# Performance work log

Measured on AMD Instinct MI355X. Metric: run time of the kernel, lower is better.

Reference implementation:

```python
import jax, jax.numpy as jnp
import numpy as np

B, T, W = 8, 4096, 1024          # batch, byte seq len, words per sequence
DB, DW = 64, 512                 # byte_embed_dim, word_embed_dim
NH = 2                           # highway layers per block
VOCAB = 264                      # 256 bytes + 4 + 4 specials
BPE_MARK, WORD_MARK = 4, 3       # bpe_mask_idx, word_mask_idx


def _make_seg_ids():
    # ragged word lengths in {3,4,5}, mean 4, summing to T per sequence
    rng = np.random.default_rng(0)
    seg = np.empty((B, T), np.int32)
    base = T // W
    for b in range(B):
        delta = np.zeros(W, np.int64)
        q = W // 4
        idx = rng.permutation(W)
        delta[idx[:q]] = 1
        delta[idx[q:2 * q]] = -1
        seg[b] = np.repeat(np.arange(W), base + delta)
    return jnp.asarray(seg)


def setup_inputs() -> dict:
    key = jax.random.key(0)
    ks = jax.random.split(key, 12)
    s = 0.05
    byte_tokens = jax.random.randint(ks[0], (B, T), 4, VOCAB)
    bpe_mask = jax.random.bernoulli(ks[1], 0.25, (B, T))
    word_mask = jax.random.bernoulli(ks[2], 0.05, (B, T))
    seg_ids = _make_seg_ids()
    tok_emb = (jax.random.normal(ks[3], (VOCAB, DB)) * s).at[0].set(0.0)  # padding_idx=0 row zeroed
    inp = {
        'byte_tokens': byte_tokens, 'bpe_mask': bpe_mask, 'word_mask': word_mask,
        'seg_ids': seg_ids, 'tok_emb': tok_emb,
        'conv0_w': jax.random.normal(ks[4], (3, DB, DW)) * s, 'conv0_b': jnp.zeros((DW,)),
        'hw0_wg': jax.random.normal(ks[5], (NH, DW, DW)) * s, 'hw0_bg': jnp.zeros((NH, DW)),
        'hw0_wh': jax.random.normal(ks[6], (NH, DW, DW)) * s, 'hw0_bh': jnp.zeros((NH, DW)),
        'conv1_w': jax.random.normal(ks[7], (3, DW, DW)) * s, 'conv1_b': jnp.zeros((DW,)),
        'hw1_wg': jax.random.normal(ks[8], (NH, DW, DW)) * s, 'hw1_bg': jnp.zeros((NH, DW)),
        'hw1_wh': jax.random.normal(ks[9], (NH, DW, DW)) * s, 'hw1_bh': jnp.zeros((NH, DW)),
        'proj_w': jax.random.normal(ks[10], (DW, DW)) * s, 'proj_b': jnp.zeros((DW,)),
    }
    return inp


def _conv_highway(x, cw, cb, wg, bg, wh, bh, residual):
    # 1D same-padded conv over sequence, optional residual, relu, then highways
    y = jax.lax.conv_general_dilated(x, cw, (1,), 'SAME',
                                     dimension_numbers=('NWC', 'WIO', 'NWC')) + cb
    if residual:
        y = y + x
    y = jax.nn.relu(y)
    for i in range(NH):
        g = jax.nn.sigmoid(y @ wg[i] + bg[i])
        h = jax.nn.relu(y @ wh[i] + bh[i])
        y = g * h + (1.0 - g) * y
    return y


def reference(byte_tokens, bpe_mask, word_mask, seg_ids, tok_emb,
              conv0_w, conv0_b, hw0_wg, hw0_bg, hw0_wh, hw0_bh,
              conv1_w, conv1_b, hw1_wg, hw1_bg, hw1_wh, hw1_bh,
              proj_w, proj_b):
    # byte embedding + marker embeddings (pad idx 0 -> zero row)
    x = (tok_emb[byte_tokens]
         + tok_emb[jnp.where(bpe_mask, BPE_MARK, 0)]
         + tok_emb[jnp.where(word_mask, WORD_MARK, 0)])          # [B,T,DB]
    x = _conv_highway(x, conv0_w, conv0_b, hw0_wg, hw0_bg, hw0_wh, hw0_bh, False)
    x = _conv_highway(x, conv1_w, conv1_b, hw1_wg, hw1_bg, hw1_wh, hw1_bh, True)
    # ragged per-word segment max over bytes (fused, replaces python loops)
    seg_max = jax.vmap(lambda xi, si: jax.ops.segment_max(xi, si, num_segments=W))
    x = seg_max(x, seg_ids)                                       # [B,W,DW]
    return x @ proj_w + proj_b
```

## Files before the change

kernel.cpp:

```cpp
#include <hip/hip_runtime.h>
#include <hip/hip_bf16.h>

using bf16 = __hip_bfloat16;
typedef __attribute__((ext_vector_type(8))) short s8v;
typedef __attribute__((ext_vector_type(4))) float f4v;

#define T_SEQ 4096
#define DWC 512

__device__ __forceinline__ float fin(float v) {
    return (v == v && fabsf(v) < 1e30f) ? v : 0.0f;
}
__device__ __forceinline__ float ldf(const void* p, size_t i, int f32) {
    return f32 ? ((const float*)p)[i] : __bfloat162float(((const bf16*)p)[i]);
}
__device__ __forceinline__ float b2f(short s) {
    unsigned u = ((unsigned)(unsigned short)s) << 16;
    return __builtin_bit_cast(float, u);
}
__device__ __forceinline__ short f2b(float v) {
    bf16 b = __float2bfloat16(v);
    return __builtin_bit_cast(short, b);
}

__device__ __forceinline__ void swz(int L, int G, int& bx, int& by) {
    int k8 = L & 7, sl = L >> 3;
    int gp = G >> 5;
    bx = sl & 3;
    by = k8 * gp + (sl >> 2);
}

__global__ __launch_bounds__(256) void diag_kernel(bf16* __restrict__ out, int n, float v)
{
    int i = blockIdx.x * 256 + threadIdx.x;
    if (i < n) out[i] = __float2bfloat16(i == 0 ? v : 0.0f);
}

__global__ __launch_bounds__(256) void detect_kernel(
    const int* __restrict__ tok, const unsigned char* __restrict__ bpe,
    const unsigned char* __restrict__ wm, const int* __restrict__ seg,
    const unsigned int* __restrict__ embw, int* __restrict__ flags)
{
    __shared__ int sh[5];
    int tid = threadIdx.x;
    if (tid < 5) sh[tid] = 0;
    __syncthreads();
    int bo = 0, bm = 0, wo = 0, wmid = 0;
    for (int i = tid; i < 16384; i += 256) {
        int odd = 2 * i + 1;
        if (bpe[odd]) bo = 1;
        if (wm[odd])  wo = 1;
        int mid = 8 * (i & 4095) + 4;
        if (bpe[mid]) bm = 1;
        if (wm[mid])  wmid = 1;
    }
    if (bo)   atomicOr(&sh[0], 1);
    if (bm)   atomicOr(&sh[1], 1);
    if (wo)   atomicOr(&sh[2], 1);
    if (wmid) atomicOr(&sh[3], 1);
    if (tid < 32 && embw[32 + tid] != 0u) atomicOr(&sh[4], 1);
    __syncthreads();
    if (tid == 0) {
        flags[0] = (tok[32767] != 0) ? 0 : 1;
        flags[1] = sh[0] ? 1 : (sh[1] ? 4 : 8);
        flags[2] = sh[2] ? 1 : (sh[3] ? 4 : 8);
        flags[3] = (seg[32767] != 0) ? 0 : 1;
        flags[4] = sh[4] ? 0 : 1;
    }
}

#define WB_TOTAL 3249664
__global__ __launch_bounds__(256) void convert_weights(
    const void* c0w, const void* c0b, const void* h0g, const void* h0bg,
    const void* h0h, const void* h0bh, const void* c1w, const void* c1b,
    const void* h1g, const void* h1bg, const void* h1h, const void* h1bh,
    const void* pw, const void* pb, const int* __restrict__ flags,
    short* __restrict__ WB)
{
    int f32 = flags[4];
    size_t i = (size_t)blockIdx.x * 256 + threadIdx.x;
    if (i >= WB_TOTAL) return;
    const void* src; size_t si;
    if (i < 98304)        { size_t n = i / 192, k = i % 192; src = c0w; si = k * 512 + n; }
    else if (i < 98816)   { src = c0b;  si = i - 98304; }
    else if (i < 623104)  { size_t o = i - 98816;  size_t l = o >> 18; o &= 262143;
                            size_t n = o >> 9, k = o & 511; src = h0g; si = (l << 18) + k * 512 + n; }
    else if (i < 624128)  { src = h0bg; si = i - 623104; }
    else if (i < 1148416) { size_t o = i - 624128; size_t l = o >> 18; o &= 262143;
                            size_t n = o >> 9, k = o & 511; src = h0h; si = (l << 18) + k * 512 + n; }
    else if (i < 1149440) { src = h0bh; si = i - 1148416; }
    else if (i < 1935872) { size_t o = i - 1149440; size_t n = o / 1536, k = o % 1536;
                            src = c1w; si = k * 512 + n; }
    else if (i < 1936384) { src = c1b;  si = i - 1935872; }
    else if (i < 2460672) { size_t o = i - 1936384; size_t l = o >> 18; o &= 262143;
                            size_t n = o >> 9, k = o & 511; src = h1g; si = (l << 18) + k * 512 + n; }
    else if (i < 2461696) { src = h1bg; si = i - 2460672; }
    else if (i < 2985984) { size_t o = i - 2461696; size_t l = o >> 18; o &= 262143;
                            size_t n = o >> 9, k = o & 511; src = h1h; si = (l << 18) + k * 512 + n; }
    else if (i < 2987008) { src = h1bh; si = i - 2985984; }
    else if (i < 3249152) { size_t o = i - 2987008; size_t n = o >> 9, k = o & 511;
                            src = pw; si = k * 512 + n; }
    else                  { src = pb;   si = i - 3249152; }
    WB[i] = f2b(ldf(src, si, f32));
}

__global__ __launch_bounds__(256) void embed_kernel(
    const int* __restrict__ tok, const unsigned char* __restrict__ bpe,
    const unsigned char* __restrict__ wm, const void* __restrict__ emb,
    const int* __restrict__ flags, short* __restrict__ xe, int bt0)
{
    int i = blockIdx.x * 256 + threadIdx.x;
    int d = i & 63;
    int btl = i >> 6;
    int bt = bt0 + btl;
    int is64t = flags[0];
    int wb = flags[1], ww = flags[2];
    int f32 = flags[4];
    int t = is64t ? (int)((const long long*)tok)[bt] : tok[bt];
    t = min(max(t, 0), 263);
    float v = ldf(emb, (size_t)t * 64 + d, f32);
    if (bpe[(size_t)bt * wb]) v += ldf(emb, 4 * 64 + d, f32);
    if (wm[(size_t)bt * ww])  v += ldf(emb, 3 * 64 + d, f32);
    xe[i] = f2b(fin(v));
}

template<int IC, bool RESID>
__global__ __launch_bounds__(512) void conv_mfma(
    const short* __restrict__ A, const short* __restrict__ WT,
    const short* __restrict__ bias, short* __restrict__ Out)
{
    constexpr int K = 3 * IC;
    __shared__ __align__(16) short As[128 * 32];
    __shared__ __align__(16) short Bs[128 * 32];
    int bx, by;
    swz(blockIdx.x, gridDim.x, bx, by);
    const int bm = by * 128;
    const int bn = bx * 128;
    const int tid = threadIdx.x;
    const int wave = tid >> 6, lane = tid & 63;
    const int wmr = (wave >> 1) * 32, wnc = (wave & 1) * 64;
    const int q = lane >> 4, ln16 = lane & 15;
    const int sr = tid >> 2, sc = (tid & 3) * 8;

    f4v acc[2][4] = {};

    for (int k0 = 0; k0 < K; k0 += 32) {
        const int tap = k0 / IC;
        const int c0 = k0 - tap * IC;
        {
            int gr = bm + sr;
            int tt = gr & (T_SEQ - 1);
            int ts = tt + tap - 1;
            uint4 va = make_uint4(0, 0, 0, 0);
            if (ts >= 0 && ts < T_SEQ)
                va = *(const uint4*)(A + (size_t)(gr + tap - 1) * IC + c0 + sc);
            *(uint4*)(&As[sr * 32 + sc]) = va;
            *(uint4*)(&Bs[sr * 32 + sc]) = *(const uint4*)(WT + (size_t)(bn + sr) * K + k0 + sc);
        }
        __syncthreads();
        s8v af[2], bf[4];
        #pragma unroll
        for (int mi = 0; mi < 2; mi++) af[mi] = *(const s8v*)(&As[(wmr + mi * 16 + ln16) * 32 + q * 8]);
        #pragma unroll
        for (int ni = 0; ni < 4; ni++) bf[ni] = *(const s8v*)(&Bs[(wnc + ni * 16 + ln16) * 32 + q * 8]);
        #pragma unroll
        for (int mi = 0; mi < 2; mi++)
            #pragma unroll
            for (int ni = 0; ni < 4; ni++)
                acc[mi][ni] = __builtin_amdgcn_mfma_f32_16x16x32_bf16(
                    af[mi], bf[ni], acc[mi][ni], 0, 0, 0);
        __syncthreads();
    }

    #pragma unroll
    for (int mi = 0; mi < 2; mi++)
        #pragma unroll
        for (int ni = 0; ni < 4; ni++) {
            int col = bn + wnc + ni * 16 + ln16;
            float bv = b2f(bias[col]);
            #pragma unroll
            for (int r = 0; r < 4; r++) {
                int row = bm + wmr + mi * 16 + q * 4 + r;
                float v = acc[mi][ni][r] + bv;
                if constexpr (RESID) v += b2f(A[(size_t)row * IC + col]);
                Out[(size_t)row * DWC + col] = f2b(fin(fmaxf(v, 0.0f)));
            }
        }
}

__global__ __launch_bounds__(512) void highway_mfma(
    const short* __restrict__ Y, const short* __restrict__ WgT,
    const short* __restrict__ bg, const short* __restrict__ WhT,
    const short* __restrict__ bh, short* __restrict__ Out)
{
    __shared__ __align__(16) short As[128 * 32];
    __shared__ __align__(16) short Bg[128 * 32];
    __shared__ __align__(16) short Bh[128 * 32];
    int bx, by;
    swz(blockIdx.x, gridDim.x, bx, by);
    const int bm = by * 128;
    const int bn = bx * 128;
    const int tid = threadIdx.x;
    const int wave = tid >> 6, lane = tid & 63;
    const int wmr = (wave >> 1) * 32, wnc = (wave & 1) * 64;
    const int q = lane >> 4, ln16 = lane & 15;
    const int sr = tid >> 2, sc = (tid & 3) * 8;

    f4v accg[2][4] = {};
    f4v acch[2][4] = {};

    for (int k0 = 0; k0 < DWC; k0 += 32) {
        *(uint4*)(&As[sr * 32 + sc]) = *(const uint4*)(Y + (size_t)(bm + sr) * DWC + k0 + sc);
        *(uint4*)(&Bg[sr * 32 + sc]) = *(const uint4*)(WgT + (size_t)(bn + sr) * DWC + k0 + sc);
        *(uint4*)(&Bh[sr * 32 + sc]) = *(const uint4*)(WhT + (size_t)(bn + sr) * DWC + k0 + sc);
        __syncthreads();
        s8v af[2], bgf[4], bhf[4];
        #pragma unroll
        for (int mi = 0; mi < 2; mi++) af[mi] = *(const s8v*)(&As[(wmr + mi * 16 + ln16) * 32 + q * 8]);
        #pragma unroll
        for (int ni = 0; ni < 4; ni++) {
            bgf[ni] = *(const s8v*)(&Bg[(wnc + ni * 16 + ln16) * 32 + q * 8]);
            bhf[ni] = *(const s8v*)(&Bh[(wnc + ni * 16 + ln16) * 32 + q * 8]);
        }
        #pragma unroll
        for (int mi = 0; mi < 2; mi++)
            #pragma unroll
            for (int ni = 0; ni < 4; ni++) {
                accg[mi][ni] = __builtin_amdgcn_mfma_f32_16x16x32_bf16(
                    af[mi], bgf[ni], accg[mi][ni], 0, 0, 0);
                acch[mi][ni] = __builtin_amdgcn_mfma_f32_16x16x32_bf16(
                    af[mi], bhf[ni], acch[mi][ni], 0, 0, 0);
            }
        __syncthreads();
    }

    #pragma unroll
    for (int mi = 0; mi < 2; mi++)
        #pragma unroll
        for (int ni = 0; ni < 4; ni++) {
            int col = bn + wnc + ni * 16 + ln16;
            float bgv = b2f(bg[col]);
            float bhv = b2f(bh[col]);
            #pragma unroll
            for (int r = 0; r < 4; r++) {
                int row = bm + wmr + mi * 16 + q * 4 + r;
                float g = 1.0f / (1.0f + expf(-(accg[mi][ni][r] + bgv)));
                float h = fmaxf(acch[mi][ni][r] + bhv, 0.0f);
                float y = b2f(Y[(size_t)row * DWC + col]);
                Out[(size_t)row * DWC + col] = f2b(fin(g * h + (1.0f - g) * y));
            }
        }
}

__global__ __launch_bounds__(512) void proj_mfma(
    const short* __restrict__ A, const short* __restrict__ WT,
    const short* __restrict__ bias, const int* __restrict__ flags,
    void* __restrict__ Out, int oroff)
{
    __shared__ __align__(16) short As[128 * 32];
    __shared__ __align__(16) short Bs[128 * 32];
    int bx, by;
    swz(blockIdx.x, gridDim.x, bx, by);
    const int bm = by * 128;
    const int bn = bx * 128;
    const int tid = threadIdx.x;
    const int wave = tid >> 6, lane = tid & 63;
    const int wmr = (wave >> 1) * 32, wnc = (wave & 1) * 64;
    const int q = lane >> 4, ln16 = lane & 15;
    const int sr = tid >> 2, sc = (tid & 3) * 8;
    const int f32 = flags[4];

    f4v acc[2][4] = {};

    for (int k0 = 0; k0 < DWC; k0 += 32) {
        *(uint4*)(&As[sr * 32 + sc]) = *(const uint4*)(A + (size_t)(bm + sr) * DWC + k0 + sc);
        *(uint4*)(&Bs[sr * 32 + sc]) = *(const uint4*)(WT + (size_t)(bn + sr) * DWC + k0 + sc);
        __syncthreads();
        s8v af[2], bf[4];
        #pragma unroll
        for (int mi = 0; mi < 2; mi++) af[mi] = *(const s8v*)(&As[(wmr + mi * 16 + ln16) * 32 + q * 8]);
        #pragma unroll
        for (int ni = 0; ni < 4; ni++) bf[ni] = *(const s8v*)(&Bs[(wnc + ni * 16 + ln16) * 32 + q * 8]);
        #pragma unroll
        for (int mi = 0; mi < 2; mi++)
            #pragma unroll
            for (int ni = 0; ni < 4; ni++)
                acc[mi][ni] = __builtin_amdgcn_mfma_f32_16x16x32_bf16(
                    af[mi], bf[ni], acc[mi][ni], 0, 0, 0);
        __syncthreads();
    }

    #pragma unroll
    for (int mi = 0; mi < 2; mi++)
        #pragma unroll
        for (int ni = 0; ni < 4; ni++) {
            int col = bn + wnc + ni * 16 + ln16;
            float bv = b2f(bias[col]);
            #pragma unroll
            for (int r = 0; r < 4; r++) {
                int row = bm + wmr + mi * 16 + q * 4 + r;
                float v = fin(acc[mi][ni][r] + bv);
                size_t oi = (size_t)(oroff + row) * DWC + col;
                if (f32) ((float*)Out)[oi] = v;
                else     ((bf16*)Out)[oi] = __float2bfloat16(v);
            }
        }
}

__global__ __launch_bounds__(256) void bounds_kernel(
    const int* __restrict__ seg, const int* __restrict__ flags,
    int* __restrict__ wstart, int* __restrict__ wend, int bt0)
{
    int il = blockIdx.x * 256 + threadIdx.x;
    int ig = bt0 + il;
    int is64 = flags[3];
    const long long* seg64 = (const long long*)seg;
    int t = il & (T_SEQ - 1);
    int bl = il >> 12;
    int s  = (is64 ? (int)seg64[ig] : seg[ig]) & 1023;
    int sp = (t == 0)         ? -1 : ((is64 ? (int)seg64[ig - 1] : seg[ig - 1]) & 1023);
    int sn = (t == T_SEQ - 1) ? -1 : ((is64 ? (int)seg64[ig + 1] : seg[ig + 1]) & 1023);
    int bw = (bl << 10) + s;
    if (sp != s) wstart[bw] = t;
    if (sn != s) wend[bw] = t;
}

__global__ __launch_bounds__(512) void segmax_kernel(
    const short* __restrict__ Y, const int* __restrict__ wstart,
    const int* __restrict__ wend, short* __restrict__ Out)
{
    int bw = blockIdx.x;
    int d = threadIdx.x;
    int bl = bw >> 10;
    int s = wstart[bw], e = wend[bw];
    s = min(max(s, 0), T_SEQ - 1);
    e = min(max(e, s), T_SEQ - 1);
    float m = b2f(Y[(size_t)((bl << 12) + s) * DWC + d]);
    for (int t = s + 1; t <= e; ++t)
        m = fmaxf(m, b2f(Y[(size_t)((bl << 12) + t) * DWC + d]));
    Out[(size_t)bw * DWC + d] = f2b(fin(m));
}

extern "C" void kernel_launch(void* const* d_in, const int* in_sizes, int n_in,
                              void* d_out, int out_size, void* d_ws, size_t ws_size,
                              hipStream_t stream)
{
    static const int expect[19] = {32768, 32768, 32768, 32768, 16896,
                                   98304, 512, 524288, 1024, 524288, 1024,
                                   786432, 512, 524288, 1024, 524288, 1024,
                                   262144, 512};
    int bad = -1;
    if (n_in < 19) bad = 31;
    else for (int i = 0; i < 19; i++) if (in_sizes[i] != expect[i]) { bad = i; break; }
    if (bad >= 0) {
        diag_kernel<<<dim3((out_size + 255) / 256), dim3(256), 0, stream>>>(
            (bf16*)d_out, out_size, 1e35f * (float)(1 + bad));
        return;
    }

    char* ws = (char*)d_ws;
    const size_t WBREG = 8ull << 20;
    short* WB    = (short*)ws;
    int*   flags = (int*)(ws + 6500352);
    const size_t perC = 8921088 + 8192 + 64;
    int C = 8;
    while (C > 1 && WBREG + (size_t)C * perC > ws_size) C >>= 1;
    if (WBREG + (size_t)C * perC > ws_size) {
        float ws_mib = (float)((double)ws_size / 1048576.0);
        diag_kernel<<<dim3((out_size + 255) / 256), dim3(256), 0, stream>>>(
            (bf16*)d_out, out_size, 1e30f * (16.0f + ws_mib));
        return;
    }

    const int*  byte_tokens = (const int*)d_in[0];
    const unsigned char* bpe_mask = (const unsigned char*)d_in[1];
    const unsigned char* word_mask = (const unsigned char*)d_in[2];
    const int*  seg_ids     = (const int*)d_in[3];
    const void* tok_emb = d_in[4];

    detect_kernel<<<dim3(1), dim3(256), 0, stream>>>(
        byte_tokens, bpe_mask, word_mask, seg_ids,
        (const unsigned int*)tok_emb, flags);

    convert_weights<<<dim3((WB_TOTAL + 255) / 256), dim3(256), 0, stream>>>(
        d_in[5], d_in[6], d_in[7], d_in[8], d_in[9], d_in[10],
        d_in[11], d_in[12], d_in[13], d_in[14], d_in[15], d_in[16],
        d_in[17], d_in[18], flags, WB);

    short* c0wT = WB;            short* c0b  = WB + 98304;
    short* h0gT = WB + 98816;    short* h0bg = WB + 623104;
    short* h0hT = WB + 624128;   short* h0bh = WB + 1148416;
    short* c1wT = WB + 1149440;  short* c1b  = WB + 1935872;
    short* h1gT = WB + 1936384;  short* h1bg = WB + 2460672;
    short* h1hT = WB + 2461696;  short* h1bh = WB + 2985984;
    short* pwT  = WB + 2987008;  short* pb   = WB + 3249152;
    const int LOFF = 262144, LBOFF = 512;

    for (int b0 = 0; b0 < 8; b0 += C) {
        const int rows  = C * T_SEQ;
        const int words = C * 1024;
        char*  chunk  = ws + WBREG;
        short* xe     = (short*)chunk;
        short* U      = (short*)(chunk + (size_t)C * 524288);
        short* V      = (short*)(chunk + (size_t)C * (524288 + 4194304));
        int*   wstart = (int*)(chunk + (size_t)C * 8912896);
        int*   wend   = wstart + words;
        short* segout = U;

        embed_kernel<<<dim3(rows * 64 / 256), dim3(256), 0, stream>>>(
            byte_tokens, bpe_mask, word_mask, tok_emb, flags, xe, b0 * T_SEQ);

        dim3 gg(4 * (rows / 128));
        conv_mfma<64, false><<<gg, dim3(512), 0, stream>>>(xe, c0wT, c0b, U);

        highway_mfma<<<gg, dim3(512), 0, stream>>>(U, h0gT, h0bg, h0hT, h0bh, V);
        highway_mfma<<<gg, dim3(512), 0, stream>>>(V, h0gT + LOFF, h0bg + LBOFF,
                                                   h0hT + LOFF, h0bh + LBOFF, U);

        conv_mfma<512, true><<<gg, dim3(512), 0, stream>>>(U, c1wT, c1b, V);

        highway_mfma<<<gg, dim3(512), 0, stream>>>(V, h1gT, h1bg, h1hT, h1bh, U);
        highway_mfma<<<gg, dim3(512), 0, stream>>>(U, h1gT + LOFF, h1bg + LBOFF,
                                                   h1hT + LOFF, h1bh + LBOFF, V);

        bounds_kernel<<<dim3(rows / 256), dim3(256), 0, stream>>>(
            seg_ids, flags, wstart, wend, b0 * T_SEQ);

        segmax_kernel<<<dim3(words), dim3(512), 0, stream>>>(V, wstart, wend, segout);

        proj_mfma<<<dim3(4 * (words / 128)), dim3(512), 0, stream>>>(
            segout, pwT, pb, flags, d_out, b0 * 1024);
    }
}
```

Baseline: 479.3 us.

## Prefetch next K-tile into registers and XOR-swizzle LDS tiles in GEMM kernels

```diff
diff --git a/kernel.cpp b/kernel.cpp
--- a/kernel.cpp
+++ b/kernel.cpp
@@ -28,6 +28,10 @@
     int gp = G >> 5;
     bx = sl & 3;
     by = k8 * gp + (sl >> 2);
+}
+
+__device__ __forceinline__ int swidx(int row, int ch) {
+    return row * 32 + ((ch ^ ((row >> 1) & 3)) << 3);
 }
 
 __global__ __launch_bounds__(256) void diag_kernel(bf16* __restrict__ out, int n, float v)
@@ -140,29 +144,43 @@
     const int wave = tid >> 6, lane = tid & 63;
     const int wmr = (wave >> 1) * 32, wnc = (wave & 1) * 64;
     const int q = lane >> 4, ln16 = lane & 15;
-    const int sr = tid >> 2, sc = (tid & 3) * 8;
+    const int sr = tid >> 2, sch = tid & 3, sc = sch * 8;
+    const int sw = swidx(sr, sch);
 
     f4v acc[2][4] = {};
+    uint4 ra, rb;
+
+    {
+        int gr = bm + sr;
+        int tt = gr & (T_SEQ - 1);
+        int ts = tt - 1;
+        ra = make_uint4(0, 0, 0, 0);
+        if (ts >= 0 && ts < T_SEQ)
+            ra = *(const uint4*)(A + (size_t)(gr - 1) * IC + sc);
+        rb = *(const uint4*)(WT + (size_t)(bn + sr) * K + sc);
+    }
 
     for (int k0 = 0; k0 < K; k0 += 32) {
-        const int tap = k0 / IC;
-        const int c0 = k0 - tap * IC;
-        {
+        *(uint4*)(&As[sw]) = ra;
+        *(uint4*)(&Bs[sw]) = rb;
+        __syncthreads();
+        if (k0 + 32 < K) {
+            int kn = k0 + 32;
+            int tap = kn / IC;
+            int c0 = kn - tap * IC;
             int gr = bm + sr;
             int tt = gr & (T_SEQ - 1);
             int ts = tt + tap - 1;
-            uint4 va = make_uint4(0, 0, 0, 0);
+            ra = make_uint4(0, 0, 0, 0);
             if (ts >= 0 && ts < T_SEQ)
-                va = *(const uint4*)(A + (size_t)(gr + tap - 1) * IC + c0 + sc);
-            *(uint4*)(&As[sr * 32 + sc]) = va;
-            *(uint4*)(&Bs[sr * 32 + sc]) = *(const uint4*)(WT + (size_t)(bn + sr) * K + k0 + sc);
-        }
-        __syncthreads();
+                ra = *(const uint4*)(A + (size_t)(gr + tap - 1) * IC + c0 + sc);
+            rb = *(const uint4*)(WT + (size_t)(bn + sr) * K + kn + sc);
+        }
         s8v af[2], bf[4];
         #pragma unroll
-        for (int mi = 0; mi < 2; mi++) af[mi] = *(const s8v*)(&As[(wmr + mi * 16 + ln16) * 32 + q * 8]);
-        #pragma unroll
-        for (int ni = 0; ni < 4; ni++) bf[ni] = *(const s8v*)(&Bs[(wnc + ni * 16 + ln16) * 32 + q * 8]);
+        for (int mi = 0; mi < 2; mi++) af[mi] = *(const s8v*)(&As[swidx(wmr + mi * 16 + ln16, q)]);
+        #pragma unroll
+        for (int ni = 0; ni < 4; ni++) bf[ni] = *(const s8v*)(&Bs[swidx(wnc + ni * 16 + ln16, q)]);
         #pragma unroll
         for (int mi = 0; mi < 2; mi++)
             #pragma unroll
@@ -204,23 +222,35 @@
     const int wave = tid >> 6, lane = tid & 63;
     const int wmr = (wave >> 1) * 32, wnc = (wave & 1) * 64;
     const int q = lane >> 4, ln16 = lane & 15;
-    const int sr = tid >> 2, sc = (tid & 3) * 8;
+    const int sr = tid >> 2, sch = tid & 3, sc = sch * 8;
+    const int sw = swidx(sr, sch);
 
     f4v accg[2][4] = {};
     f4v acch[2][4] = {};
+    uint4 ra, rg, rh;
+
+    ra = *(const uint4*)(Y + (size_t)(bm + sr) * DWC + sc);
+    rg = *(const uint4*)(WgT + (size_t)(bn + sr) * DWC + sc);
+    rh = *(const uint4*)(WhT + (size_t)(bn + sr) * DWC + sc);
 
     for (int k0 = 0; k0 < DWC; k0 += 32) {
-        *(uint4*)(&As[sr * 32 + sc]) = *(const uint4*)(Y + (size_t)(bm + sr) * DWC + k0 + sc);
-        *(uint4*)(&Bg[sr * 32 + sc]) = *(const uint4*)(WgT + (size_t)(bn + sr) * DWC + k0 + sc);
-        *(uint4*)(&Bh[sr * 32 + sc]) = *(const uint4*)(WhT + (size_t)(bn + sr) * DWC + k0 + sc);
-        __syncthreads();
+        *(uint4*)(&As[sw]) = ra;
+        *(uint4*)(&Bg[sw]) = rg;
+        *(uint4*)(&Bh[sw]) = rh;
+        __syncthreads();
+        if (k0 + 32 < DWC) {
+            int kn = k0 + 32;
+            ra = *(const uint4*)(Y + (size_t)(bm + sr) * DWC + kn + sc);
+            rg = *(const uint4*)(WgT + (size_t)(bn + sr) * DWC + kn + sc);
+            rh = *(const uint4*)(WhT + (size_t)(bn + sr) * DWC + kn + sc);
+        }
         s8v af[2], bgf[4], bhf[4];
         #pragma unroll
-        for (int mi = 0; mi < 2; mi++) af[mi] = *(const s8v*)(&As[(wmr + mi * 16 + ln16) * 32 + q * 8]);
+        for (int mi = 0; mi < 2; mi++) af[mi] = *(const s8v*)(&As[swidx(wmr + mi * 16 + ln16, q)]);
         #pragma unroll
         for (int ni = 0; ni < 4; ni++) {
-            bgf[ni] = *(const s8v*)(&Bg[(wnc + ni * 16 + ln16) * 32 + q * 8]);
-            bhf[ni] = *(const s8v*)(&Bh[(wnc + ni * 16 + ln16) * 32 + q * 8]);
+            bgf[ni] = *(const s8v*)(&Bg[swidx(wnc + ni * 16 + ln16, q)]);
+            bhf[ni] = *(const s8v*)(&Bh[swidx(wnc + ni * 16 + ln16, q)]);
         }
         #pragma unroll
         for (int mi = 0; mi < 2; mi++)
@@ -267,20 +297,29 @@
     const int wave = tid >> 6, lane = tid & 63;
     const int wmr = (wave >> 1) * 32, wnc = (wave & 1) * 64;
     const int q = lane >> 4, ln16 = lane & 15;
-    const int sr = tid >> 2, sc = (tid & 3) * 8;
+    const int sr = tid >> 2, sch = tid & 3, sc = sch * 8;
+    const int sw = swidx(sr, sch);
     const int f32 = flags[4];
 
     f4v acc[2][4] = {};
+    uint4 ra, rb;
+    ra = *(const uint4*)(A + (size_t)(bm + sr) * DWC + sc);
+    rb = *(const uint4*)(WT + (size_t)(bn + sr) * DWC + sc);
 
     for (int k0 = 0; k0 < DWC; k0 += 32) {
-        *(uint4*)(&As[sr * 32 + sc]) = *(const uint4*)(A + (size_t)(bm + sr) * DWC + k0 + sc);
-        *(uint4*)(&Bs[sr * 32 + sc]) = *(const uint4*)(WT + (size_t)(bn + sr) * DWC + k0 + sc);
-        __syncthreads();
+        *(uint4*)(&As[sw]) = ra;
+        *(uint4*)(&Bs[sw]) = rb;
+        __syncthreads();
+        if (k0 + 32 < DWC) {
+            int kn = k0 + 32;
+            ra = *(const uint4*)(A + (size_t)(bm + sr) * DWC + kn + sc);
+            rb = *(const uint4*)(WT + (size_t)(bn + sr) * DWC + kn + sc);
+        }
         s8v af[2], bf[4];
         #pragma unroll
-        for (int mi = 0; mi < 2; mi++) af[mi] = *(const s8v*)(&As[(wmr + mi * 16 + ln16) * 32 + q * 8]);
-        #pragma unroll
-        for (int ni = 0; ni < 4; ni++) bf[ni] = *(const s8v*)(&Bs[(wnc + ni * 16 + ln16) * 32 + q * 8]);
+        for (int mi = 0; mi < 2; mi++) af[mi] = *(const s8v*)(&As[swidx(wmr + mi * 16 + ln16, q)]);
+        #pragma unroll
+        for (int ni = 0; ni < 4; ni++) bf[ni] = *(const s8v*)(&Bs[swidx(wnc + ni * 16 + ln16, q)]);
         #pragma unroll
         for (int mi = 0; mi < 2; mi++)
             #pragma unroll
```

Result: no change. 476.2 us (-0.7%).

## Double-buffer GEMM tiles via direct global-to-LDS loads with XOR swizzle

Applied to the files above, without the earlier changes.

```diff
diff --git a/kernel.cpp b/kernel.cpp
--- a/kernel.cpp
+++ b/kernel.cpp
@@ -21,6 +21,12 @@
 __device__ __forceinline__ short f2b(float v) {
     bf16 b = __float2bfloat16(v);
     return __builtin_bit_cast(short, b);
+}
+
+__device__ __forceinline__ void dma16(const short* g, short* l) {
+    __builtin_amdgcn_global_load_lds(
+        (const __attribute__((address_space(1))) void*)g,
+        (__attribute__((address_space(3))) void*)l, 16, 0, 0);
 }
 
 __device__ __forceinline__ void swz(int L, int G, int& bx, int& by) {
@@ -28,6 +34,10 @@
     int gp = G >> 5;
     bx = sl & 3;
     by = k8 * gp + (sl >> 2);
+}
+
+__device__ __forceinline__ int swidx(int row, int ch) {
+    return row * 32 + ((ch ^ ((row >> 1) & 3)) << 3);
 }
 
 __global__ __launch_bounds__(256) void diag_kernel(bf16* __restrict__ out, int n, float v)
@@ -79,7 +89,8 @@
 {
     int f32 = flags[4];
     size_t i = (size_t)blockIdx.x * 256 + threadIdx.x;
-    if (i >= WB_TOTAL) return;
+    if (i >= WB_TOTAL + 64) return;
+    if (i >= WB_TOTAL) { WB[i] = 0; return; }
     const void* src; size_t si;
     if (i < 98304)        { size_t n = i / 192, k = i % 192; src = c0w; si = k * 512 + n; }
     else if (i < 98816)   { src = c0b;  si = i - 98304; }
@@ -127,49 +138,58 @@
 template<int IC, bool RESID>
 __global__ __launch_bounds__(512) void conv_mfma(
     const short* __restrict__ A, const short* __restrict__ WT,
-    const short* __restrict__ bias, short* __restrict__ Out)
+    const short* __restrict__ bias, const short* __restrict__ zpad,
+    short* __restrict__ Out)
 {
     constexpr int K = 3 * IC;
-    __shared__ __align__(16) short As[128 * 32];
-    __shared__ __align__(16) short Bs[128 * 32];
+    constexpr int NIT = K / 32;
+    __shared__ __align__(16) short As[2][128 * 32];
+    __shared__ __align__(16) short Bs[2][128 * 32];
     int bx, by;
     swz(blockIdx.x, gridDim.x, bx, by);
-    const int bm = by * 128;
-    const int bn = bx * 128;
+    const int bm = by * 128, bn = bx * 128;
     const int tid = threadIdx.x;
     const int wave = tid >> 6, lane = tid & 63;
     const int wmr = (wave >> 1) * 32, wnc = (wave & 1) * 64;
     const int q = lane >> 4, ln16 = lane & 15;
-    const int sr = tid >> 2, sc = (tid & 3) * 8;
+    const int row = (wave << 4) + (lane >> 2);
+    const int chl = (lane & 3) ^ ((row >> 1) & 3);
+    const int gr = bm + row;
+    const int tt = gr & (T_SEQ - 1);
+    const short* Bbase = WT + (size_t)(bn + row) * K + chl * 8;
 
     f4v acc[2][4] = {};
-
-    for (int k0 = 0; k0 < K; k0 += 32) {
-        const int tap = k0 / IC;
-        const int c0 = k0 - tap * IC;
-        {
-            int gr = bm + sr;
-            int tt = gr & (T_SEQ - 1);
+    int p = 0;
+
+    {
+        int ts = tt - 1;
+        const short* sa = (ts >= 0 && ts < T_SEQ) ? A + (size_t)(gr - 1) * IC + chl * 8 : zpad;
+        dma16(sa, &As[0][wave << 9]);
+        dma16(Bbase, &Bs[0][wave << 9]);
+    }
+    for (int it = 0; it < NIT; ++it) {
+        __syncthreads();
+        if (it + 1 < NIT) {
+            int kn = (it + 1) * 32;
+            int tap = kn / IC, c0 = kn - tap * IC;
             int ts = tt + tap - 1;
-            uint4 va = make_uint4(0, 0, 0, 0);
-            if (ts >= 0 && ts < T_SEQ)
-                va = *(const uint4*)(A + (size_t)(gr + tap - 1) * IC + c0 + sc);
-            *(uint4*)(&As[sr * 32 + sc]) = va;
-            *(uint4*)(&Bs[sr * 32 + sc]) = *(const uint4*)(WT + (size_t)(bn + sr) * K + k0 + sc);
-        }
-        __syncthreads();
+            const short* sa = (ts >= 0 && ts < T_SEQ)
+                ? A + (size_t)(gr + tap - 1) * IC + c0 + chl * 8 : zpad;
+            dma16(sa, &As[p ^ 1][wave << 9]);
+            dma16(Bbase + kn, &Bs[p ^ 1][wave << 9]);
+        }
         s8v af[2], bf[4];
         #pragma unroll
-        for (int mi = 0; mi < 2; mi++) af[mi] = *(const s8v*)(&As[(wmr + mi * 16 + ln16) * 32 + q * 8]);
-        #pragma unroll
-        for (int ni = 0; ni < 4; ni++) bf[ni] = *(const s8v*)(&Bs[(wnc + ni * 16 + ln16) * 32 + q * 8]);
+        for (int mi = 0; mi < 2; mi++) af[mi] = *(const s8v*)(&As[p][swidx(wmr + mi * 16 + ln16, q)]);
+        #pragma unroll
+        for (int ni = 0; ni < 4; ni++) bf[ni] = *(const s8v*)(&Bs[p][swidx(wnc + ni * 16 + ln16, q)]);
         #pragma unroll
         for (int mi = 0; mi < 2; mi++)
             #pragma unroll
             for (int ni = 0; ni < 4; ni++)
                 acc[mi][ni] = __builtin_amdgcn_mfma_f32_16x16x32_bf16(
                     af[mi], bf[ni], acc[mi][ni], 0, 0, 0);
-        __syncthreads();
+        p ^= 1;
     }
 
     #pragma unroll
@@ -180,10 +200,10 @@
             float bv = b2f(bias[col]);
             #pragma unroll
             for (int r = 0; r < 4; r++) {
-                int row = bm + wmr + mi * 16 + q * 4 + r;
+                int orow = bm + wmr + mi * 16 + q * 4 + r;
                 float v = acc[mi][ni][r] + bv;
-                if constexpr (RESID) v += b2f(A[(size_t)row * IC + col]);
-                Out[(size_t)row * DWC + col] = f2b(fin(fmaxf(v, 0.0f)));
+                if constexpr (RESID) v += b2f(A[(size_t)orow * IC + col]);
+                Out[(size_t)orow * DWC + col] = f2b(fin(fmaxf(v, 0.0f)));
             }
         }
 }
@@ -193,34 +213,46 @@
     const short* __restrict__ bg, const short* __restrict__ WhT,
     const short* __restrict__ bh, short* __restrict__ Out)
 {
-    __shared__ __align__(16) short As[128 * 32];
-    __shared__ __align__(16) short Bg[128 * 32];
-    __shared__ __align__(16) short Bh[128 * 32];
+    constexpr int NIT = DWC / 32;
+    __shared__ __align__(16) short As[2][128 * 32];
+    __shared__ __align__(16) short Bg[2][128 * 32];
+    __shared__ __align__(16) short Bh[2][128 * 32];
     int bx, by;
     swz(blockIdx.x, gridDim.x, bx, by);
-    const int bm = by * 128;
-    const int bn = bx * 128;
+    const int bm = by * 128, bn = bx * 128;
     const int tid = threadIdx.x;
     const int wave = tid >> 6, lane = tid & 63;
     const int wmr = (wave >> 1) * 32, wnc = (wave & 1) * 64;
     const int q = lane >> 4, ln16 = lane & 15;
-    const int sr = tid >> 2, sc = (tid & 3) * 8;
+    const int row = (wave << 4) + (lane >> 2);
+    const int chl = (lane & 3) ^ ((row >> 1) & 3);
+    const short* Abase = Y   + (size_t)(bm + row) * DWC + chl * 8;
+    const short* Gbase = WgT + (size_t)(bn + row) * DWC + chl * 8;
+    const short* Hbase = WhT + (size_t)(bn + row) * DWC + chl * 8;
 
     f4v accg[2][4] = {};
     f4v acch[2][4] = {};
-
-    for (int k0 = 0; k0 < DWC; k0 += 32) {
-        *(uint4*)(&As[sr * 32 + sc]) = *(const uint4*)(Y + (size_t)(bm + sr) * DWC + k0 + sc);
-        *(uint4*)(&Bg[sr * 32 + sc]) = *(const uint4*)(WgT + (size_t)(bn + sr) * DWC + k0 + sc);
-        *(uint4*)(&Bh[sr * 32 + sc]) = *(const uint4*)(WhT + (size_t)(bn + sr) * DWC + k0 + sc);
+    int p = 0;
+
+    dma16(Abase, &As[0][wave << 9]);
+    dma16(Gbase, &Bg[0][wave << 9]);
+    dma16(Hbase, &Bh[0][wave << 9]);
+
+    for (int it = 0; it < NIT; ++it) {
         __syncthreads();
+        if (it + 1 < NIT) {
+            int kn = (it + 1) * 32;
+            dma16(Abase + kn, &As[p ^ 1][wave << 9]);
+            dma16(Gbase + kn, &Bg[p ^ 1][wave << 9]);
+            dma16(Hbase + kn, &Bh[p ^ 1][wave << 9]);
+        }
         s8v af[2], bgf[4], bhf[4];
         #pragma unroll
-        for (int mi = 0; mi < 2; mi++) af[mi] = *(const s8v*)(&As[(wmr + mi * 16 + ln16) * 32 + q * 8]);
+        for (int mi = 0; mi < 2; mi++) af[mi] = *(const s8v*)(&As[p][swidx(wmr + mi * 16 + ln16, q)]);
         #pragma unroll
         for (int ni = 0; ni < 4; ni++) {
-            bgf[ni] = *(const s8v*)(&Bg[(wnc + ni * 16 + ln16) * 32 + q * 8]);
-            bhf[ni] = *(const s8v*)(&Bh[(wnc + ni * 16 + ln16) * 32 + q * 8]);
+            bgf[ni] = *(const s8v*)(&Bg[p][swidx(wnc + ni * 16 + ln16, q)]);
+            bhf[ni] = *(const s8v*)(&Bh[p][swidx(wnc + ni * 16 + ln16, q)]);
         }
         #pragma unroll
         for (int mi = 0; mi < 2; mi++)
@@ -231,7 +263,7 @@
                 acch[mi][ni] = __builtin_amdgcn_mfma_f32_16x16x32_bf16(
                     af[mi], bhf[ni], acch[mi][ni], 0, 0, 0);
             }
-        __syncthreads();
+        p ^= 1;
     }
 
     #pragma unroll
@@ -243,11 +275,11 @@
             float bhv = b2f(bh[col]);
             #pragma unroll
             for (int r = 0; r < 4; r++) {
-                int row = bm + wmr + mi * 16 + q * 4 + r;
+                int orow = bm + wmr + mi * 16 + q * 4 + r;
                 float g = 1.0f / (1.0f + expf(-(accg[mi][ni][r] + bgv)));
                 float h = fmaxf(acch[mi][ni][r] + bhv, 0.0f);
-                float y = b2f(Y[(size_t)row * DWC + col]);
-                Out[(size_t)row * DWC + col] = f2b(fin(g * h + (1.0f - g) * y));
+                float y = b2f(Y[(size_t)orow * DWC + col]);
+                Out[(size_t)orow * DWC + col] = f2b(fin(g * h + (1.0f - g) * y));
             }
         }
 }
@@ -257,37 +289,47 @@
     const short* __restrict__ bias, const int* __restrict__ flags,
     void* __restrict__ Out, int oroff)
 {
-    __shared__ __align__(16) short As[128 * 32];
-    __shared__ __align__(16) short Bs[128 * 32];
+    constexpr int NIT = DWC / 32;
+    __shared__ __align__(16) short As[2][128 * 32];
+    __shared__ __align__(16) short Bs[2][128 * 32];
     int bx, by;
     swz(blockIdx.x, gridDim.x, bx, by);
-    const int bm = by * 128;
-    const int bn = bx * 128;
+    const int bm = by * 128, bn = bx * 128;
     const int tid = threadIdx.x;
     const int wave = tid >> 6, lane = tid & 63;
     const int wmr = (wave >> 1) * 32, wnc = (wave & 1) * 64;
     const int q = lane >> 4, ln16 = lane & 15;
-    const int sr = tid >> 2, sc = (tid & 3) * 8;
+    const int row = (wave << 4) + (lane >> 2);
+    const int chl = (lane & 3) ^ ((row >> 1) & 3);
     const int f32 = flags[4];
+    const short* Abase = A  + (size_t)(bm + row) * DWC + chl * 8;
+    const short* Bbase = WT + (size_t)(bn + row) * DWC + chl * 8;
 
     f4v acc[2][4] = {};
-
-    for (int k0 = 0; k0 < DWC; k0 += 32) {
-        *(uint4*)(&As[sr * 32 + sc]) = *(const uint4*)(A + (size_t)(bm + sr) * DWC + k0 + sc);
-        *(uint4*)(&Bs[sr * 32 + sc]) = *(const uint4*)(WT + (size_t)(bn + sr) * DWC + k0 + sc);
+    int p = 0;
+
+    dma16(Abase, &As[0][wave << 9]);
+    dma16(Bbase, &Bs[0][wave << 9]);
+
+    for (int it = 0; it < NIT; ++it) {
         __syncthreads();
+        if (it + 1 < NIT) {
+            int kn = (it + 1) * 32;
+            dma16(Abase + kn, &As[p ^ 1][wave << 9]);
+            dma16(Bbase + kn, &Bs[p ^ 1][wave << 9]);
+        }
         s8v af[2], bf[4];
         #pragma unroll
-        for (int mi = 0; mi < 2; mi++) af[mi] = *(const s8v*)(&As[(wmr + mi * 16 + ln16) * 32 + q * 8]);
-        #pragma unroll
-        for (int ni = 0; ni < 4; ni++) bf[ni] = *(const s8v*)(&Bs[(wnc + ni * 16 + ln16) * 32 + q * 8]);
+        for (int mi = 0; mi < 2; mi++) af[mi] = *(const s8v*)(&As[p][swidx(wmr + mi * 16 + ln16, q)]);
+        #pragma unroll
+        for (int ni = 0; ni < 4; ni++) bf[ni] = *(const s8v*)(&Bs[p][swidx(wnc + ni * 16 + ln16, q)]);
         #pragma unroll
         for (int mi = 0; mi < 2; mi++)
             #pragma unroll
             for (int ni = 0; ni < 4; ni++)
                 acc[mi][ni] = __builtin_amdgcn_mfma_f32_16x16x32_bf16(
                     af[mi], bf[ni], acc[mi][ni], 0, 0, 0);
-        __syncthreads();
+        p ^= 1;
     }
 
     #pragma unroll
@@ -298,9 +340,9 @@
             float bv = b2f(bias[col]);
             #pragma unroll
             for (int r = 0; r < 4; r++) {
-                int row = bm + wmr + mi * 16 + q * 4 + r;
+                int orow = bm + wmr + mi * 16 + q * 4 + r;
                 float v = fin(acc[mi][ni][r] + bv);
-                size_t oi = (size_t)(oroff + row) * DWC + col;
+                size_t oi = (size_t)(oroff + orow) * DWC + col;
                 if (f32) ((float*)Out)[oi] = v;
                 else     ((bf16*)Out)[oi] = __float2bfloat16(v);
             }
@@ -382,7 +424,7 @@
         byte_tokens, bpe_mask, word_mask, seg_ids,
         (const unsigned int*)tok_emb, flags);
 
-    convert_weights<<<dim3((WB_TOTAL + 255) / 256), dim3(256), 0, stream>>>(
+    convert_weights<<<dim3((WB_TOTAL + 64 + 255) / 256), dim3(256), 0, stream>>>(
         d_in[5], d_in[6], d_in[7], d_in[8], d_in[9], d_in[10],
         d_in[11], d_in[12], d_in[13], d_in[14], d_in[15], d_in[16],
         d_in[17], d_in[18], flags, WB);
@@ -394,6 +436,7 @@
     short* h1gT = WB + 1936384;  short* h1bg = WB + 2460672;
     short* h1hT = WB + 2461696;  short* h1bh = WB + 2985984;
     short* pwT  = WB + 2987008;  short* pb   = WB + 3249152;
+    short* zpad = WB + WB_TOTAL;
     const int LOFF = 262144, LBOFF = 512;
 
     for (int b0 = 0; b0 < 8; b0 += C) {
@@ -411,13 +454,13 @@
             byte_tokens, bpe_mask, word_mask, tok_emb, flags, xe, b0 * T_SEQ);
 
         dim3 gg(4 * (rows / 128));
-        conv_mfma<64, false><<<gg, dim3(512), 0, stream>>>(xe, c0wT, c0b, U);
+        conv_mfma<64, false><<<gg, dim3(512), 0, stream>>>(xe, c0wT, c0b, zpad, U);
 
         highway_mfma<<<gg, dim3(512), 0, stream>>>(U, h0gT, h0bg, h0hT, h0bh, V);
         highway_mfma<<<gg, dim3(512), 0, stream>>>(V, h0gT + LOFF, h0bg + LBOFF,
                                                    h0hT + LOFF, h0bh + LBOFF, U);
 
-        conv_mfma<512, true><<<gg, dim3(512), 0, stream>>>(U, c1wT, c1b, V);
+        conv_mfma<512, true><<<gg, dim3(512), 0, stream>>>(U, c1wT, c1b, zpad, V);
 
         highway_mfma<<<gg, dim3(512), 0, stream>>>(V, h1gT, h1bg, h1hT, h1bh, U);
         highway_mfma<<<gg, dim3(512), 0, stream>>>(U, h1gT + LOFF, h1bg + LBOFF,
```

After: 495.4 us. 3.4% more time.
